# Optimization experiments

Hardware: AMD Instinct MI355X
Metric: run time of the kernel (lower is better)

The kernel has to match this reference:

```python
import jax, jax.numpy as jnp
import numpy as np
import math

L = 12      # n_layer (alternating adaptive True/False)
H = 8       # n_head
C = 256     # n_embd
DH = C // H # head dim = 32
BS = 828    # block_size
T = 827     # seq len after dropping last token
VOCAB = 16384
CAM = 30
IMG = 256


def get_sinusoid(n_position, d_hid):
    pos = np.arange(n_position)[:, None].astype(np.float64)
    hid = np.arange(d_hid)[None, :]
    angle = pos / np.power(10000.0, 2.0 * (hid // 2) / d_hid)
    table = np.zeros_like(angle)
    table[:, 0::2] = np.sin(angle[:, 0::2])
    table[:, 1::2] = np.cos(angle[:, 1::2])
    return jnp.asarray(table[None], jnp.float32)  # [1, n_position, d_hid]


def layer_norm(x, w, b):
    m = x.mean(-1, keepdims=True)
    v = ((x - m) ** 2).mean(-1, keepdims=True)
    return (x - m) * jax.lax.rsqrt(v + 1e-5) * w + b


def setup_inputs() -> dict:
    key = jax.random.key(0)
    ks = iter(jax.random.split(key, 64))
    nrm = lambda shape, s=1.0: jax.random.normal(next(ks), shape, jnp.float32) * s
    B = 4
    inp = {
        'dc_emb': nrm((B, 572, C)),
        'z_emb': nrm((B, 256, C)),
        'p1': nrm((B, CAM)),
        'p2': nrm((B, CAM)),
        'p3': nrm((B, CAM)),
        'frame_emb': nrm((1, 256, C), 0.02),
        'camera_emb': nrm((1, 30, C), 0.02),
        'time_emb': get_sinusoid(BS, C),
        'loc_W1': nrm((2 * CAM, CAM), 0.02), 'loc_b1': jnp.zeros((2 * CAM,)),
        'loc_W2': nrm((IMG * IMG, 2 * CAM), 0.02), 'loc_b2': jnp.zeros((IMG * IMG,)),
        'ln1_w': jnp.ones((L, C)), 'ln1_b': jnp.zeros((L, C)),
        'Wq': nrm((L, C, C), 0.02), 'bq': jnp.zeros((L, C)),
        'Wk': nrm((L, C, C), 0.02), 'bk': jnp.zeros((L, C)),
        'Wv': nrm((L, C, C), 0.02), 'bv': jnp.zeros((L, C)),
        'Wo': nrm((L, C, C), 0.02), 'bo': jnp.zeros((L, C)),
        'ln2_w': jnp.ones((L, C)), 'ln2_b': jnp.zeros((L, C)),
        'W1': nrm((L, 4 * C, C), 0.02), 'b1': jnp.zeros((L, 4 * C)),
        'W2': nrm((L, C, 4 * C), 0.02), 'b2': jnp.zeros((L, C)),
        'lnf_w': jnp.ones((C,)), 'lnf_b': jnp.zeros((C,)),
        'head_W': nrm((VOCAB, C), 0.02),
    }
    return inp


def _forward(dc_emb, z_emb, p1, p2, p3, frame_emb, camera_emb, time_emb,
             loc_W1, loc_b1, loc_W2, loc_b2,
             ln1_w, ln1_b, Wq, bq, Wk, bk, Wv, bv, Wo, bo,
             ln2_w, ln2_b, W1, b1, W2, b2, lnf_w, lnf_b, head_W):
    B = dc_emb.shape[0]
    scale = 1.0 / math.sqrt(DH)

    # AdaptiveAttention bias h: [B, 1, BS, BS] with three 256x256 learned blocks
    def locality(p):
        z = jax.nn.gelu(p @ loc_W1.T + loc_b1, approximate=False)
        z = z @ loc_W2.T + loc_b2
        return z.reshape(B, IMG, IMG)

    h = jnp.zeros((B, 1, BS, BS), dc_emb.dtype)
    h = h.at[:, 0, 285:541, 0:256].set(locality(p1))
    h = h.at[:, 0, 571:827, 0:256].set(locality(p2))
    h = h.at[:, 0, 571:827, 286:542].set(locality(p3))
    h = h[:, :, :T, :T]

    # token + role + time embeddings
    tok = jnp.concatenate([dc_emb, z_emb], axis=1)[:, :-1, :]  # [B, T, C]
    role = jnp.concatenate([frame_emb, camera_emb, frame_emb, camera_emb, frame_emb], axis=1)[:, :T, :]
    x = tok + role + time_emb[:, :T, :]

    causal = jnp.tril(jnp.ones((T, T), bool))  # [T, T]

    for i in range(L):
        adaptive = (i % 2 == 0)
        xn = layer_norm(x, ln1_w[i], ln1_b[i])
        q = (xn @ Wq[i].T + bq[i]).reshape(B, T, H, DH)
        k = (xn @ Wk[i].T + bk[i]).reshape(B, T, H, DH)
        v = (xn @ Wv[i].T + bv[i]).reshape(B, T, H, DH)
        att = jnp.einsum('bqhd,bkhd->bhqk', q, k) * scale
        if adaptive:
            att = att + h
        att = jnp.where(causal, att, -jnp.inf)
        att = jax.nn.softmax(att, axis=-1)
        y = jnp.einsum('bhqk,bkhd->bqhd', att, v).reshape(B, T, C)
        x = x + y @ Wo[i].T + bo[i]
        xn2 = layer_norm(x, ln2_w[i], ln2_b[i])
        x = x + jax.nn.gelu(xn2 @ W1[i].T + b1[i], approximate=False) @ W2[i].T + b2[i]

    x = layer_norm(x, lnf_w, lnf_b)
    logits = x @ head_W.T  # [B, T, VOCAB]
    return logits


def reference(dc_emb, z_emb, p1, p2, p3, frame_emb, camera_emb, time_emb,
              loc_W1, loc_b1, loc_W2, loc_b2,
              ln1_w, ln1_b, Wq, bq, Wk, bk, Wv, bv, Wo, bo,
              ln2_w, ln2_b, W1, b1, W2, b2, lnf_w, lnf_b, head_W):
    return _forward(dc_emb, z_emb, p1, p2, p3, frame_emb, camera_emb, time_emb,
                    loc_W1, loc_b1, loc_W2, loc_b2,
                    ln1_w, ln1_b, Wq, bq, Wk, bk, Wv, bv, Wo, bo,
                    ln2_w, ln2_b, W1, b1, W2, b2, lnf_w, lnf_b, head_W)
```

## Files before the change

### kernel.cpp

```cpp
#include <hip/hip_runtime.h>
#include <hip/hip_bf16.h>
#include <math.h>

#define T_LEN 827
#define M_ROWS 3308
#define NLAYER 12

typedef __attribute__((ext_vector_type(4))) float f32x4;
typedef __attribute__((ext_vector_type(8))) short bf16x8;

__device__ __forceinline__ float gelu_f(float x) {
    return 0.5f * x * (1.0f + erff(x * 0.70710678118654752440f));
}

__device__ __forceinline__ short f2bf_s(float x) {
    __hip_bfloat16 h = __float2bfloat16(x);
    return *reinterpret_cast<short*>(&h);
}

__global__ void cvt_kernel(const float* __restrict__ in, __hip_bfloat16* __restrict__ out, int n4) {
    int i = blockIdx.x * blockDim.x + threadIdx.x;
    if (i >= n4) return;
    float4 v = reinterpret_cast<const float4*>(in)[i];
    out[4*i+0] = __float2bfloat16(v.x);
    out[4*i+1] = __float2bfloat16(v.y);
    out[4*i+2] = __float2bfloat16(v.z);
    out[4*i+3] = __float2bfloat16(v.w);
}

__global__ void prep_wqkv_kernel(const float* __restrict__ Wq, const float* __restrict__ Wk,
                                 const float* __restrict__ Wv, __hip_bfloat16* __restrict__ out) {
    int i = blockIdx.x * 256 + threadIdx.x;
    if (i >= 12*768*64) return;
    int el = i * 4;
    int layer = el / (768*256);
    int rem = el % (768*256);
    int row = rem >> 8, col = rem & 255;
    const float* src;
    float sc = 1.f;
    if (row < 256)      { src = Wq + ((size_t)layer*256 + row)*256 + col; sc = 0.17677669529663687f; }
    else if (row < 512) { src = Wk + ((size_t)layer*256 + (row-256))*256 + col; }
    else                { src = Wv + ((size_t)layer*256 + (row-512))*256 + col; }
    float4 v = *reinterpret_cast<const float4*>(src);
    out[el+0] = __float2bfloat16(v.x * sc);
    out[el+1] = __float2bfloat16(v.y * sc);
    out[el+2] = __float2bfloat16(v.z * sc);
    out[el+3] = __float2bfloat16(v.w * sc);
}

__global__ void prep_bqkv_kernel(const float* __restrict__ bq, const float* __restrict__ bk,
                                 const float* __restrict__ bv, float* __restrict__ out) {
    int i = blockIdx.x * 256 + threadIdx.x;
    if (i >= 12*768) return;
    int layer = i / 768, row = i % 768;
    float v;
    if (row < 256)      v = bq[layer*256 + row] * 0.17677669529663687f;
    else if (row < 512) v = bk[layer*256 + (row-256)];
    else                v = bv[layer*256 + (row-512)];
    out[i] = v;
}

__global__ void zero_kernel(float* __restrict__ p, int n) {
    for (int i = blockIdx.x * blockDim.x + threadIdx.x; i < n; i += gridDim.x * blockDim.x)
        p[i] = 0.f;
}

__global__ void loc_z1_kernel(const float* __restrict__ p1, const float* __restrict__ p2,
                              const float* __restrict__ p3, const float* __restrict__ W1,
                              const float* __restrict__ b1, float* __restrict__ z1) {
    for (int i = threadIdx.x; i < 720; i += 256) {
        int pi = i / 240, rem = i % 240, b = rem / 60, j = rem % 60;
        const float* p = (pi == 0) ? p1 : ((pi == 1) ? p2 : p3);
        float acc = b1[j];
        #pragma unroll
        for (int c = 0; c < 30; ++c) acc += p[b*30 + c] * W1[j*30 + c];
        z1[i] = gelu_f(acc);
    }
}

__global__ void h_fill_kernel(const float* __restrict__ z1, const float* __restrict__ W2,
                              const float* __restrict__ b2, float* __restrict__ h) {
    __shared__ float z[720];
    int tid = threadIdx.x;
    for (int i = tid; i < 720; i += 256) z[i] = z1[i];
    __syncthreads();
    int j = blockIdx.x * 256 + tid;
    float w[60];
    #pragma unroll
    for (int c = 0; c < 60; ++c) w[c] = W2[(size_t)j*60 + c];
    float bj = b2[j];
    int r = j >> 8, cc = j & 255;
    const int br[3] = {285, 571, 571};
    const int bc[3] = {0, 0, 286};
    #pragma unroll
    for (int pi = 0; pi < 3; ++pi) {
        for (int b = 0; b < 4; ++b) {
            float acc = bj;
            #pragma unroll
            for (int c = 0; c < 60; ++c) acc += z[pi*240 + b*60 + c] * w[c];
            h[(size_t)b*T_LEN*T_LEN + (size_t)(br[pi] + r)*T_LEN + bc[pi] + cc] = acc;
        }
    }
}

__global__ void init_x_kernel(const float* __restrict__ dc, const float* __restrict__ z,
                              const float* __restrict__ frame, const float* __restrict__ cam,
                              const float* __restrict__ timeE, float* __restrict__ x) {
    int idx = blockIdx.x * 256 + threadIdx.x;
    int m = idx >> 8, c = idx & 255;
    int b = m / T_LEN, t = m % T_LEN;
    float tok = (t < 572) ? dc[((size_t)b*572 + t)*256 + c]
                          : z[((size_t)b*256 + (t - 572))*256 + c];
    float role;
    if      (t < 256) role = frame[t*256 + c];
    else if (t < 286) role = cam[(t-256)*256 + c];
    else if (t < 542) role = frame[(t-286)*256 + c];
    else if (t < 572) role = cam[(t-542)*256 + c];
    else              role = frame[(t-572)*256 + c];
    x[idx] = tok + role + timeE[t*256 + c];
}

template<bool LN, bool RESID, bool OUTBF16>
__global__ __launch_bounds__(256) void gemm_k256(
    const float* __restrict__ xsrc, const float* __restrict__ lnw, const float* __restrict__ lnb,
    const __hip_bfloat16* __restrict__ Abf,
    const __hip_bfloat16* __restrict__ W, const float* __restrict__ bias,
    const float* __restrict__ resid, void* __restrict__ out, int M, int N)
{
    __shared__ __hip_bfloat16 As[64][264];
    __shared__ __hip_bfloat16 Bs[64][264];
    __shared__ float redS[4][64], redQ[4][64];
    const int tid = threadIdx.x;
    const int m0 = blockIdx.x * 64, n0 = blockIdx.y * 64;
    const int r = tid >> 2, sg = tid & 3;

    {
        const __hip_bfloat16* bsrc = W + (size_t)(n0 + r) * 256 + sg * 8;
        #pragma unroll
        for (int j = 0; j < 8; ++j)
            *reinterpret_cast<uint4*>(&Bs[r][sg*8 + j*32]) =
                *reinterpret_cast<const uint4*>(bsrc + j*32);
    }
    int gr = m0 + r; if (gr > M-1) gr = M-1;
    if constexpr (LN) {
        const float* src = xsrc + (size_t)gr * 256;
        float s = 0.f, q = 0.f;
        #pragma unroll
        for (int j = 0; j < 8; ++j) {
            int k = sg*8 + j*32;
            float4 a = *reinterpret_cast<const float4*>(src + k);
            float4 c4 = *reinterpret_cast<const float4*>(src + k + 4);
            s += a.x + a.y + a.z + a.w + c4.x + c4.y + c4.z + c4.w;
            q += a.x*a.x + a.y*a.y + a.z*a.z + a.w*a.w
               + c4.x*c4.x + c4.y*c4.y + c4.z*c4.z + c4.w*c4.w;
        }
        redS[sg][r] = s; redQ[sg][r] = q;
        __syncthreads();
        float mean = (redS[0][r] + redS[1][r] + redS[2][r] + redS[3][r]) * (1.f/256.f);
        float msq  = (redQ[0][r] + redQ[1][r] + redQ[2][r] + redQ[3][r]) * (1.f/256.f);
        float rstd = rsqrtf(msq - mean*mean + 1e-5f);
        #pragma unroll
        for (int j = 0; j < 8; ++j) {
            int k = sg*8 + j*32;
            float4 a = *reinterpret_cast<const float4*>(src + k);
            float4 c4 = *reinterpret_cast<const float4*>(src + k + 4);
            float v[8] = {a.x, a.y, a.z, a.w, c4.x, c4.y, c4.z, c4.w};
            bf16x8 pk;
            #pragma unroll
            for (int e = 0; e < 8; ++e)
                pk[e] = f2bf_s((v[e] - mean) * rstd * lnw[k+e] + lnb[k+e]);
            *reinterpret_cast<bf16x8*>(&As[r][k]) = pk;
        }
    } else {
        const __hip_bfloat16* asrc = Abf + (size_t)gr * 256 + sg * 8;
        #pragma unroll
        for (int j = 0; j < 8; ++j)
            *reinterpret_cast<uint4*>(&As[r][sg*8 + j*32]) =
                *reinterpret_cast<const uint4*>(asrc + j*32);
    }
    __syncthreads();

    const int wid = tid >> 6, lane = tid & 63;
    const int wm = wid >> 1, wn = wid & 1, c = lane & 15, g = lane >> 4;
    f32x4 acc[2][2];
    #pragma unroll
    for (int mi = 0; mi < 2; ++mi)
        #pragma unroll
        for (int ni = 0; ni < 2; ++ni)
            acc[mi][ni] = (f32x4){0.f, 0.f, 0.f, 0.f};

    #pragma unroll
    for (int kj = 0; kj < 8; ++kj) {
        bf16x8 a0 = *reinterpret_cast<const bf16x8*>(&As[wm*32 + c][kj*32 + g*8]);
        bf16x8 a1 = *reinterpret_cast<const bf16x8*>(&As[wm*32 + 16 + c][kj*32 + g*8]);
        bf16x8 b0 = *reinterpret_cast<const bf16x8*>(&Bs[wn*32 + c][kj*32 + g*8]);
        bf16x8 b1v = *reinterpret_cast<const bf16x8*>(&Bs[wn*32 + 16 + c][kj*32 + g*8]);
        acc[0][0] = __builtin_amdgcn_mfma_f32_16x16x32_bf16(a0, b0, acc[0][0], 0, 0, 0);
        acc[0][1] = __builtin_amdgcn_mfma_f32_16x16x32_bf16(a0, b1v, acc[0][1], 0, 0, 0);
        acc[1][0] = __builtin_amdgcn_mfma_f32_16x16x32_bf16(a1, b0, acc[1][0], 0, 0, 0);
        acc[1][1] = __builtin_amdgcn_mfma_f32_16x16x32_bf16(a1, b1v, acc[1][1], 0, 0, 0);
    }

    #pragma unroll
    for (int mi = 0; mi < 2; ++mi) {
        #pragma unroll
        for (int ni = 0; ni < 2; ++ni) {
            int n = n0 + wn*32 + ni*16 + c;
            float bb = bias ? bias[n] : 0.f;
            #pragma unroll
            for (int rg = 0; rg < 4; ++rg) {
                int m = m0 + wm*32 + mi*16 + g*4 + rg;
                if (m >= M) continue;
                float v = acc[mi][ni][rg] + bb;
                if (RESID) v += resid[(size_t)m*N + n];
                if (OUTBF16) ((__hip_bfloat16*)out)[(size_t)m*N + n] = __float2bfloat16(v);
                else         ((float*)out)[(size_t)m*N + n] = v;
            }
        }
    }
}

template<bool FINAL>
__global__ __launch_bounds__(512) void mlp_fused(
    float* __restrict__ x,
    const float* __restrict__ ln2w, const float* __restrict__ ln2b,
    const __hip_bfloat16* __restrict__ W1, const float* __restrict__ b1,
    const __hip_bfloat16* __restrict__ W2, const float* __restrict__ b2,
    const float* __restrict__ lnfw, const float* __restrict__ lnfb,
    __hip_bfloat16* __restrict__ xn)
{
    __shared__ __hip_bfloat16 As[32][264];
    __shared__ __hip_bfloat16 Ms[32][1044];
    const int tid = threadIdx.x;
    const int m0 = blockIdx.x * 32;
    const int w = tid >> 6, lane = tid & 63, c = lane & 15, g = lane >> 4;

    {
        int r = tid >> 4, p = tid & 15;
        int gr = m0 + r; if (gr > M_ROWS-1) gr = M_ROWS-1;
        const float* src = x + (size_t)gr*256 + p*16;
        float4 f0 = *reinterpret_cast<const float4*>(src);
        float4 f1 = *reinterpret_cast<const float4*>(src + 4);
        float4 f2 = *reinterpret_cast<const float4*>(src + 8);
        float4 f3 = *reinterpret_cast<const float4*>(src + 12);
        float vv[16] = {f0.x,f0.y,f0.z,f0.w, f1.x,f1.y,f1.z,f1.w,
                        f2.x,f2.y,f2.z,f2.w, f3.x,f3.y,f3.z,f3.w};
        float s = 0.f, q = 0.f;
        #pragma unroll
        for (int e = 0; e < 16; ++e) { s += vv[e]; q += vv[e]*vv[e]; }
        #pragma unroll
        for (int msk = 1; msk <= 8; msk <<= 1) { s += __shfl_xor(s, msk); q += __shfl_xor(q, msk); }
        float mean = s * (1.f/256.f);
        float rstd = rsqrtf(q*(1.f/256.f) - mean*mean + 1e-5f);
        bf16x8 pk0, pk1;
        #pragma unroll
        for (int e = 0; e < 8; ++e) {
            pk0[e] = f2bf_s((vv[e]   - mean)*rstd*ln2w[p*16+e]   + ln2b[p*16+e]);
            pk1[e] = f2bf_s((vv[8+e] - mean)*rstd*ln2w[p*16+8+e] + ln2b[p*16+8+e]);
        }
        *reinterpret_cast<bf16x8*>(&As[r][p*16])     = pk0;
        *reinterpret_cast<bf16x8*>(&As[r][p*16 + 8]) = pk1;
    }
    __syncthreads();

    #pragma unroll 1
    for (int ns = 0; ns < 8; ++ns) {
        int nb = w*128 + ns*16;
        const __hip_bfloat16* wrow = W1 + (size_t)(nb + c)*256 + g*8;
        f32x4 a0 = (f32x4){0.f,0.f,0.f,0.f}, a1 = (f32x4){0.f,0.f,0.f,0.f};
        #pragma unroll
        for (int kj = 0; kj < 8; ++kj) {
            bf16x8 bfrag = *reinterpret_cast<const bf16x8*>(wrow + kj*32);
            bf16x8 af0 = *reinterpret_cast<const bf16x8*>(&As[c][kj*32 + g*8]);
            bf16x8 af1 = *reinterpret_cast<const bf16x8*>(&As[16 + c][kj*32 + g*8]);
            a0 = __builtin_amdgcn_mfma_f32_16x16x32_bf16(af0, bfrag, a0, 0, 0, 0);
            a1 = __builtin_amdgcn_mfma_f32_16x16x32_bf16(af1, bfrag, a1, 0, 0, 0);
        }
        float bb = b1[nb + c];
        #pragma unroll
        for (int rg = 0; rg < 4; ++rg) {
            Ms[g*4 + rg][nb + c]      = __float2bfloat16(gelu_f(a0[rg] + bb));
            Ms[16 + g*4 + rg][nb + c] = __float2bfloat16(gelu_f(a1[rg] + bb));
        }
    }
    __syncthreads();

    f32x4 o[2][2];
    #pragma unroll
    for (int i = 0; i < 2; ++i)
        #pragma unroll
        for (int j = 0; j < 2; ++j)
            o[i][j] = (f32x4){0.f,0.f,0.f,0.f};
    #pragma unroll
    for (int ns2 = 0; ns2 < 2; ++ns2) {
        int nb = w*32 + ns2*16;
        const __hip_bfloat16* wrow = W2 + (size_t)(nb + c)*1024 + g*8;
        #pragma unroll
        for (int kj = 0; kj < 32; ++kj) {
            bf16x8 bfrag = *reinterpret_cast<const bf16x8*>(wrow + kj*32);
            bf16x8 af0 = *reinterpret_cast<const bf16x8*>(&Ms[c][kj*32 + g*8]);
            bf16x8 af1 = *reinterpret_cast<const bf16x8*>(&Ms[16 + c][kj*32 + g*8]);
            o[ns2][0] = __builtin_amdgcn_mfma_f32_16x16x32_bf16(af0, bfrag, o[ns2][0], 0, 0, 0);
            o[ns2][1] = __builtin_amdgcn_mfma_f32_16x16x32_bf16(af1, bfrag, o[ns2][1], 0, 0, 0);
        }
    }
    __syncthreads();

    float* xf = reinterpret_cast<float*>(&Ms[0][0]);
    #pragma unroll
    for (int ns2 = 0; ns2 < 2; ++ns2) {
        int nb = w*32 + ns2*16;
        float bb = b2[nb + c];
        #pragma unroll
        for (int mi = 0; mi < 2; ++mi) {
            #pragma unroll
            for (int rg = 0; rg < 4; ++rg) {
                int row = mi*16 + g*4 + rg;
                int gm = m0 + row;
                if (gm < M_ROWS) {
                    float v = o[ns2][mi][rg] + bb + x[(size_t)gm*256 + nb + c];
                    x[(size_t)gm*256 + nb + c] = v;
                    if (FINAL) xf[row*256 + nb + c] = v;
                }
            }
        }
    }

    if constexpr (FINAL) {
        __syncthreads();
        int r = tid >> 4, p = tid & 15;
        int gm = m0 + r;
        const float* src = xf + r*256 + p*16;
        float4 f0 = *reinterpret_cast<const float4*>(src);
        float4 f1 = *reinterpret_cast<const float4*>(src + 4);
        float4 f2 = *reinterpret_cast<const float4*>(src + 8);
        float4 f3 = *reinterpret_cast<const float4*>(src + 12);
        float vv[16] = {f0.x,f0.y,f0.z,f0.w, f1.x,f1.y,f1.z,f1.w,
                        f2.x,f2.y,f2.z,f2.w, f3.x,f3.y,f3.z,f3.w};
        float s = 0.f, q = 0.f;
        #pragma unroll
        for (int e = 0; e < 16; ++e) { s += vv[e]; q += vv[e]*vv[e]; }
        #pragma unroll
        for (int msk = 1; msk <= 8; msk <<= 1) { s += __shfl_xor(s, msk); q += __shfl_xor(q, msk); }
        float mean = s * (1.f/256.f);
        float rstd = rsqrtf(q*(1.f/256.f) - mean*mean + 1e-5f);
        if (gm < M_ROWS) {
            bf16x8 pk0, pk1;
            #pragma unroll
            for (int e = 0; e < 8; ++e) {
                pk0[e] = f2bf_s((vv[e]   - mean)*rstd*lnfw[p*16+e]   + lnfb[p*16+e]);
                pk1[e] = f2bf_s((vv[8+e] - mean)*rstd*lnfw[p*16+8+e] + lnfb[p*16+8+e]);
            }
            *reinterpret_cast<bf16x8*>(&xn[(size_t)gm*256 + p*16])     = pk0;
            *reinterpret_cast<bf16x8*>(&xn[(size_t)gm*256 + p*16 + 8]) = pk1;
        }
    }
}

template<int ADAPT>
__global__ __launch_bounds__(256) void attn_mfma_kernel(const __hip_bfloat16* __restrict__ qkv,
                                                        const float* __restrict__ hbuf,
                                                        __hip_bfloat16* __restrict__ y) {
    const int qi = blockIdx.x, hh = blockIdx.y, b = blockIdx.z;
    const int tid = threadIdx.x;
    const int w = tid >> 6, lane = tid & 63;
    const int c = lane & 15, g = lane >> 4;
    const int q0 = qi * 64;
    const int qw0 = q0 + w * 16;

    __shared__ short Ks[2][64][40];
    __shared__ short Vt[2][32][68];
    __shared__ short Pw[4][16][72];

    int qrow = qw0 + c; if (qrow > T_LEN-1) qrow = T_LEN-1;
    bf16x8 aq = *reinterpret_cast<const bf16x8*>(qkv + ((size_t)b*T_LEN + qrow)*768 + hh*32 + g*8);

    float m_r[4] = {-INFINITY, -INFINITY, -INFINITY, -INFINITY};
    float l_r[4] = {0.f, 0.f, 0.f, 0.f};
    f32x4 acc[2];
    acc[0] = (f32x4){0.f,0.f,0.f,0.f};
    acc[1] = (f32x4){0.f,0.f,0.f,0.f};

    const int nk = min(q0 + 64, T_LEN);
    const int nit = (nk + 63) >> 6;
    const int srow = tid >> 2;
    const int scol8 = (tid & 3) * 8;

    bf16x8 kreg, vreg;
    {
        int krow = srow; if (krow > T_LEN-1) krow = T_LEN-1;
        const __hip_bfloat16* base = qkv + ((size_t)b*T_LEN + krow)*768 + hh*32 + scol8;
        kreg = *reinterpret_cast<const bf16x8*>(base + 256);
        vreg = *reinterpret_cast<const bf16x8*>(base + 512);
    }

    for (int it = 0; it < nit; ++it) {
        const int bsel = it & 1;
        const int kb = it * 64;
        *reinterpret_cast<bf16x8*>(&Ks[bsel][srow][scol8]) = kreg;
        #pragma unroll
        for (int jj = 0; jj < 8; ++jj) Vt[bsel][scol8 + jj][srow] = vreg[jj];
        __syncthreads();
        if (it + 1 < nit) {
            int krow = kb + 64 + srow; if (krow > T_LEN-1) krow = T_LEN-1;
            const __hip_bfloat16* base = qkv + ((size_t)b*T_LEN + krow)*768 + hh*32 + scol8;
            kreg = *reinterpret_cast<const bf16x8*>(base + 256);
            vreg = *reinterpret_cast<const bf16x8*>(base + 512);
        }

        f32x4 sc4[4];
        #pragma unroll
        for (int j = 0; j < 4; ++j) {
            bf16x8 bk = *reinterpret_cast<const bf16x8*>(&Ks[bsel][j*16 + c][g*8]);
            sc4[j] = __builtin_amdgcn_mfma_f32_16x16x32_bf16(aq, bk, (f32x4){0.f,0.f,0.f,0.f}, 0, 0, 0);
        }

        float sv[4][4];
        #pragma unroll
        for (int j = 0; j < 4; ++j) {
            int kk = kb + j*16 + c;
            #pragma unroll
            for (int rg = 0; rg < 4; ++rg) {
                int qq = qw0 + g*4 + rg;
                bool valid = (qq < T_LEN) && (kk <= qq);
                float s = sc4[j][rg];
                if (ADAPT) s += valid ? hbuf[((size_t)b*T_LEN + qq)*T_LEN + kk] : 0.f;
                sv[j][rg] = valid ? s : -INFINITY;
            }
        }

        float sf[4];
        #pragma unroll
        for (int rg = 0; rg < 4; ++rg) {
            float m = fmaxf(fmaxf(sv[0][rg], sv[1][rg]), fmaxf(sv[2][rg], sv[3][rg]));
            #pragma unroll
            for (int msk = 1; msk <= 8; msk <<= 1) m = fmaxf(m, __shfl_xor(m, msk));
            float mn = fmaxf(m_r[rg], m);
            sf[rg] = __expf(m_r[rg] - mn);
            m_r[rg] = mn;
        }
        float p[4][4];
        #pragma unroll
        for (int rg = 0; rg < 4; ++rg) {
            float su = 0.f;
            #pragma unroll
            for (int j = 0; j < 4; ++j) {
                float e = __expf(sv[j][rg] - m_r[rg]);
                p[j][rg] = e;
                su += e;
            }
            #pragma unroll
            for (int msk = 1; msk <= 8; msk <<= 1) su += __shfl_xor(su, msk);
            l_r[rg] = l_r[rg] * sf[rg] + su;
            acc[0][rg] *= sf[rg];
            acc[1][rg] *= sf[rg];
        }

        #pragma unroll
        for (int j = 0; j < 4; ++j)
            #pragma unroll
            for (int rg = 0; rg < 4; ++rg)
                Pw[w][g*4 + rg][j*16 + c] = f2bf_s(p[j][rg]);

        #pragma unroll
        for (int kc = 0; kc < 2; ++kc) {
            bf16x8 ap = *reinterpret_cast<const bf16x8*>(&Pw[w][c][kc*32 + g*8]);
            #pragma unroll
            for (int dt = 0; dt < 2; ++dt) {
                bf16x8 bv = *reinterpret_cast<const bf16x8*>(&Vt[bsel][dt*16 + c][kc*32 + g*8]);
                acc[dt] = __builtin_amdgcn_mfma_f32_16x16x32_bf16(ap, bv, acc[dt], 0, 0, 0);
            }
        }
    }

    #pragma unroll
    for (int rg = 0; rg < 4; ++rg) {
        int qq = qw0 + g*4 + rg;
        if (qq >= T_LEN) continue;
        float inv = 1.f / l_r[rg];
        #pragma unroll
        for (int dt = 0; dt < 2; ++dt)
            y[((size_t)b*T_LEN + qq)*256 + hh*32 + dt*16 + c] = __float2bfloat16(acc[dt][rg] * inv);
    }
}

extern "C" void kernel_launch(void* const* d_in, const int* in_sizes, int n_in,
                              void* d_out, int out_size, void* d_ws, size_t ws_size,
                              hipStream_t stream) {
    const float* dc    = (const float*)d_in[0];
    const float* zemb  = (const float*)d_in[1];
    const float* p1    = (const float*)d_in[2];
    const float* p2    = (const float*)d_in[3];
    const float* p3    = (const float*)d_in[4];
    const float* frame = (const float*)d_in[5];
    const float* cam   = (const float*)d_in[6];
    const float* timeE = (const float*)d_in[7];
    const float* locW1 = (const float*)d_in[8];
    const float* locb1 = (const float*)d_in[9];
    const float* locW2 = (const float*)d_in[10];
    const float* locb2 = (const float*)d_in[11];
    const float* ln1w  = (const float*)d_in[12];
    const float* ln1b  = (const float*)d_in[13];
    const float* Wq    = (const float*)d_in[14];
    const float* bq    = (const float*)d_in[15];
    const float* Wk    = (const float*)d_in[16];
    const float* bk    = (const float*)d_in[17];
    const float* Wv    = (const float*)d_in[18];
    const float* bv    = (const float*)d_in[19];
    const float* Wo    = (const float*)d_in[20];
    const float* bo    = (const float*)d_in[21];
    const float* ln2w  = (const float*)d_in[22];
    const float* ln2b  = (const float*)d_in[23];
    const float* W1p   = (const float*)d_in[24];
    const float* b1p   = (const float*)d_in[25];
    const float* W2p   = (const float*)d_in[26];
    const float* b2p   = (const float*)d_in[27];
    const float* lnfw  = (const float*)d_in[28];
    const float* lnfb  = (const float*)d_in[29];
    const float* headW = (const float*)d_in[30];

    char* wsb = (char*)d_ws;
    size_t off = 0;
    auto alloc = [&](size_t bytes) -> char* {
        char* p = wsb + off;
        off += (bytes + 255) & ~(size_t)255;
        return p;
    };
    __hip_bfloat16* wqkv_bf = (__hip_bfloat16*)alloc(12ull*768*256*2);
    float*          bqkv    = (float*)alloc(12ull*768*4);
    __hip_bfloat16* wo_bf = (__hip_bfloat16*)alloc(12ull*65536*2);
    __hip_bfloat16* w1_bf = (__hip_bfloat16*)alloc(12ull*262144*2);
    __hip_bfloat16* w2_bf = (__hip_bfloat16*)alloc(12ull*262144*2);
    __hip_bfloat16* wh_bf = (__hip_bfloat16*)alloc(16384ull*256*2);
    float* hbuf = (float*)alloc(4ull*T_LEN*T_LEN*4);
    float* x    = (float*)alloc((size_t)M_ROWS*256*4);
    __hip_bfloat16* xn   = (__hip_bfloat16*)alloc((size_t)M_ROWS*256*2);
    __hip_bfloat16* qkvb = (__hip_bfloat16*)alloc((size_t)M_ROWS*768*2);
    __hip_bfloat16* yb   = (__hip_bfloat16*)alloc((size_t)M_ROWS*256*2);
    float* z1   = (float*)alloc(720*4);

    prep_wqkv_kernel<<<(12*768*64 + 255)/256, 256, 0, stream>>>(Wq, Wk, Wv, wqkv_bf);
    prep_bqkv_kernel<<<36, 256, 0, stream>>>(bq, bk, bv, bqkv);
    cvt_kernel<<<768, 256, 0, stream>>>(Wo, wo_bf, 196608);
    cvt_kernel<<<3072, 256, 0, stream>>>(W1p, w1_bf, 786432);
    cvt_kernel<<<3072, 256, 0, stream>>>(W2p, w2_bf, 786432);
    cvt_kernel<<<4096, 256, 0, stream>>>(headW, wh_bf, 1048576);

    loc_z1_kernel<<<1, 256, 0, stream>>>(p1, p2, p3, locW1, locb1, z1);
    zero_kernel<<<2048, 256, 0, stream>>>(hbuf, 4*T_LEN*T_LEN);
    h_fill_kernel<<<256, 256, 0, stream>>>(z1, locW2, locb2, hbuf);

    init_x_kernel<<<M_ROWS, 256, 0, stream>>>(dc, zemb, frame, cam, timeE, x);

    dim3 gqkv(52, 12);
    dim3 goproj(52, 4);
    dim3 gattn(13, 8, 4);

    for (int i = 0; i < NLAYER; ++i) {
        gemm_k256<true,false,true><<<gqkv, 256, 0, stream>>>(
            x, ln1w + i*256, ln1b + i*256, nullptr,
            wqkv_bf + (size_t)i*196608, bqkv + i*768, nullptr, qkvb, M_ROWS, 768);
        if (i % 2 == 0) attn_mfma_kernel<1><<<gattn, 256, 0, stream>>>(qkvb, hbuf, yb);
        else            attn_mfma_kernel<0><<<gattn, 256, 0, stream>>>(qkvb, hbuf, yb);
        gemm_k256<false,true,false><<<goproj, 256, 0, stream>>>(
            nullptr, nullptr, nullptr, yb,
            wo_bf + (size_t)i*65536, bo + i*256, x, x, M_ROWS, 256);
        if (i == NLAYER-1)
            mlp_fused<true><<<104, 512, 0, stream>>>(
                x, ln2w + i*256, ln2b + i*256,
                w1_bf + (size_t)i*262144, b1p + i*1024,
                w2_bf + (size_t)i*262144, b2p + i*256, lnfw, lnfb, xn);
        else
            mlp_fused<false><<<104, 512, 0, stream>>>(
                x, ln2w + i*256, ln2b + i*256,
                w1_bf + (size_t)i*262144, b1p + i*1024,
                w2_bf + (size_t)i*262144, b2p + i*256, nullptr, nullptr, nullptr);
    }

    gemm_k256<false,false,false><<<dim3(52, 256), 256, 0, stream>>>(
        nullptr, nullptr, nullptr, xn, wh_bf, nullptr, nullptr, (float*)d_out, M_ROWS, 16384);
}
```

Measured before the change: 1.183 ms.

## Split attention along keys with merge pass, store bias in bf16, fuse next-layer LN

Attention is split into key chunks of up to 256 keys (28 work items per batch-head instead of 13 query blocks). Each chunk writes partial outputs and running max/sum, and a separate merge kernel combines them, which is meant to balance causal work and raise occupancy. The adaptive bias buffer is stored in bf16 to halve its memory traffic. The MLP kernel now always emits the next layer's LN1-normalised bf16 activations, so the QKV GEMM no longer recomputes layernorm. The cost is an extra launch per layer, fp32 partial round-trips through memory, and bf16 rounding of the bias.

```diff
diff --git a/kernel.cpp b/kernel.cpp
--- a/kernel.cpp
+++ b/kernel.cpp
@@ -79,7 +79,7 @@
 }
 
 __global__ void h_fill_kernel(const float* __restrict__ z1, const float* __restrict__ W2,
-                              const float* __restrict__ b2, float* __restrict__ h) {
+                              const float* __restrict__ b2, __hip_bfloat16* __restrict__ h) {
     __shared__ float z[720];
     int tid = threadIdx.x;
     for (int i = tid; i < 720; i += 256) z[i] = z1[i];
@@ -98,7 +98,7 @@
             float acc = bj;
             #pragma unroll
             for (int c = 0; c < 60; ++c) acc += z[pi*240 + b*60 + c] * w[c];
-            h[(size_t)b*T_LEN*T_LEN + (size_t)(br[pi] + r)*T_LEN + bc[pi] + cc] = acc;
+            h[(size_t)b*T_LEN*T_LEN + (size_t)(br[pi] + r)*T_LEN + bc[pi] + cc] = __float2bfloat16(acc);
         }
     }
 }
@@ -120,6 +120,31 @@
     x[idx] = tok + role + timeE[t*256 + c];
 }
 
+__global__ __launch_bounds__(256) void ln_kernel(const float* __restrict__ x,
+                                                 const float* __restrict__ w,
+                                                 const float* __restrict__ b,
+                                                 __hip_bfloat16* __restrict__ out) {
+    int row = blockIdx.x, tid = threadIdx.x;
+    float v = x[(size_t)row*256 + tid];
+    float s = v;
+    #pragma unroll
+    for (int off = 32; off; off >>= 1) s += __shfl_down(s, off);
+    __shared__ float red[4];
+    if ((tid & 63) == 0) red[tid >> 6] = s;
+    __syncthreads();
+    float mean = (red[0] + red[1] + red[2] + red[3]) * (1.f/256.f);
+    float d = v - mean;
+    float s2 = d * d;
+    #pragma unroll
+    for (int off = 32; off; off >>= 1) s2 += __shfl_down(s2, off);
+    __shared__ float red2[4];
+    if ((tid & 63) == 0) red2[tid >> 6] = s2;
+    __syncthreads();
+    float var = (red2[0] + red2[1] + red2[2] + red2[3]) * (1.f/256.f);
+    float rs = rsqrtf(var + 1e-5f);
+    out[(size_t)row*256 + tid] = __float2bfloat16(d * rs * w[tid] + b[tid]);
+}
+
 template<bool LN, bool RESID, bool OUTBF16>
 __global__ __launch_bounds__(256) void gemm_k256(
     const float* __restrict__ xsrc, const float* __restrict__ lnw, const float* __restrict__ lnb,
@@ -220,13 +245,12 @@
     }
 }
 
-template<bool FINAL>
 __global__ __launch_bounds__(512) void mlp_fused(
     float* __restrict__ x,
     const float* __restrict__ ln2w, const float* __restrict__ ln2b,
     const __hip_bfloat16* __restrict__ W1, const float* __restrict__ b1,
     const __hip_bfloat16* __restrict__ W2, const float* __restrict__ b2,
-    const float* __restrict__ lnfw, const float* __restrict__ lnfb,
+    const float* __restrict__ lnow, const float* __restrict__ lnob,
     __hip_bfloat16* __restrict__ xn)
 {
     __shared__ __hip_bfloat16 As[32][264];
@@ -320,14 +344,14 @@
                 if (gm < M_ROWS) {
                     float v = o[ns2][mi][rg] + bb + x[(size_t)gm*256 + nb + c];
                     x[(size_t)gm*256 + nb + c] = v;
-                    if (FINAL) xf[row*256 + nb + c] = v;
+                    xf[row*256 + nb + c] = v;
                 }
             }
         }
     }
-
-    if constexpr (FINAL) {
-        __syncthreads();
+    __syncthreads();
+
+    {
         int r = tid >> 4, p = tid & 15;
         int gm = m0 + r;
         const float* src = xf + r*256 + p*16;
@@ -348,8 +372,8 @@
             bf16x8 pk0, pk1;
             #pragma unroll
             for (int e = 0; e < 8; ++e) {
-                pk0[e] = f2bf_s((vv[e]   - mean)*rstd*lnfw[p*16+e]   + lnfb[p*16+e]);
-                pk1[e] = f2bf_s((vv[8+e] - mean)*rstd*lnfw[p*16+8+e] + lnfb[p*16+8+e]);
+                pk0[e] = f2bf_s((vv[e]   - mean)*rstd*lnow[p*16+e]   + lnob[p*16+e]);
+                pk1[e] = f2bf_s((vv[8+e] - mean)*rstd*lnow[p*16+8+e] + lnob[p*16+8+e]);
             }
             *reinterpret_cast<bf16x8*>(&xn[(size_t)gm*256 + p*16])     = pk0;
             *reinterpret_cast<bf16x8*>(&xn[(size_t)gm*256 + p*16 + 8]) = pk1;
@@ -358,14 +382,28 @@
 }
 
 template<int ADAPT>
-__global__ __launch_bounds__(256) void attn_mfma_kernel(const __hip_bfloat16* __restrict__ qkv,
-                                                        const float* __restrict__ hbuf,
-                                                        __hip_bfloat16* __restrict__ y) {
-    const int qi = blockIdx.x, hh = blockIdx.y, b = blockIdx.z;
+__global__ __launch_bounds__(256) void attn_split_kernel(const __hip_bfloat16* __restrict__ qkv,
+                                                         const __hip_bfloat16* __restrict__ hbuf,
+                                                         float* __restrict__ pacc,
+                                                         float* __restrict__ pml) {
+    const int fi = blockIdx.x, hh = blockIdx.y, b = blockIdx.z;
+    int qi = 0;
+    while (qi < 12) {
+        int n1 = qi + 1;
+        int bn = n1 + (n1 > 4 ? n1 - 4 : 0) + (n1 > 8 ? n1 - 8 : 0);
+        if (fi < bn) break;
+        ++qi;
+    }
+    const int base = qi + (qi > 4 ? qi - 4 : 0) + (qi > 8 ? qi - 8 : 0);
+    const int ck = fi - base;
+    const int q0 = qi * 64;
+    const int kstart = ck * 256;
+    const int kend = min(q0 + 64, T_LEN);
+    const int nit = min(4, (kend - kstart + 63) >> 6);
+
     const int tid = threadIdx.x;
     const int w = tid >> 6, lane = tid & 63;
     const int c = lane & 15, g = lane >> 4;
-    const int q0 = qi * 64;
     const int qw0 = q0 + w * 16;
 
     __shared__ short Ks[2][64][40];
@@ -381,31 +419,29 @@
     acc[0] = (f32x4){0.f,0.f,0.f,0.f};
     acc[1] = (f32x4){0.f,0.f,0.f,0.f};
 
-    const int nk = min(q0 + 64, T_LEN);
-    const int nit = (nk + 63) >> 6;
     const int srow = tid >> 2;
     const int scol8 = (tid & 3) * 8;
 
     bf16x8 kreg, vreg;
     {
-        int krow = srow; if (krow > T_LEN-1) krow = T_LEN-1;
-        const __hip_bfloat16* base = qkv + ((size_t)b*T_LEN + krow)*768 + hh*32 + scol8;
-        kreg = *reinterpret_cast<const bf16x8*>(base + 256);
-        vreg = *reinterpret_cast<const bf16x8*>(base + 512);
+        int krow = kstart + srow; if (krow > T_LEN-1) krow = T_LEN-1;
+        const __hip_bfloat16* gbase = qkv + ((size_t)b*T_LEN + krow)*768 + hh*32 + scol8;
+        kreg = *reinterpret_cast<const bf16x8*>(gbase + 256);
+        vreg = *reinterpret_cast<const bf16x8*>(gbase + 512);
     }
 
     for (int it = 0; it < nit; ++it) {
         const int bsel = it & 1;
-        const int kb = it * 64;
+        const int kb = kstart + it * 64;
         *reinterpret_cast<bf16x8*>(&Ks[bsel][srow][scol8]) = kreg;
         #pragma unroll
         for (int jj = 0; jj < 8; ++jj) Vt[bsel][scol8 + jj][srow] = vreg[jj];
         __syncthreads();
         if (it + 1 < nit) {
             int krow = kb + 64 + srow; if (krow > T_LEN-1) krow = T_LEN-1;
-            const __hip_bfloat16* base = qkv + ((size_t)b*T_LEN + krow)*768 + hh*32 + scol8;
-            kreg = *reinterpret_cast<const bf16x8*>(base + 256);
-            vreg = *reinterpret_cast<const bf16x8*>(base + 512);
+            const __hip_bfloat16* gbase = qkv + ((size_t)b*T_LEN + krow)*768 + hh*32 + scol8;
+            kreg = *reinterpret_cast<const bf16x8*>(gbase + 256);
+            vreg = *reinterpret_cast<const bf16x8*>(gbase + 512);
         }
 
         f32x4 sc4[4];
@@ -424,7 +460,7 @@
                 int qq = qw0 + g*4 + rg;
                 bool valid = (qq < T_LEN) && (kk <= qq);
                 float s = sc4[j][rg];
-                if (ADAPT) s += valid ? hbuf[((size_t)b*T_LEN + qq)*T_LEN + kk] : 0.f;
+                if (ADAPT) s += valid ? __bfloat162float(hbuf[((size_t)b*T_LEN + qq)*T_LEN + kk]) : 0.f;
                 sv[j][rg] = valid ? s : -INFINITY;
             }
         }
@@ -473,14 +509,43 @@
         }
     }
 
+    const int slot = (b*8 + hh)*28 + fi;
+    float* paccs = pacc + (size_t)slot * 2048;
     #pragma unroll
     for (int rg = 0; rg < 4; ++rg) {
-        int qq = qw0 + g*4 + rg;
+        int row = w*16 + g*4 + rg;
+        paccs[row*32 + c]      = acc[0][rg];
+        paccs[row*32 + 16 + c] = acc[1][rg];
+        if (c == 0) {
+            pml[(size_t)slot*128 + row*2]     = m_r[rg];
+            pml[(size_t)slot*128 + row*2 + 1] = l_r[rg];
+        }
+    }
+}
+
+__global__ __launch_bounds__(256) void attn_merge_kernel(const float* __restrict__ pacc,
+                                                         const float* __restrict__ pml,
+                                                         __hip_bfloat16* __restrict__ y) {
+    const int qi = blockIdx.x, hh = blockIdx.y, b = blockIdx.z;
+    const int nc = qi/4 + 1;
+    const int base = qi + (qi > 4 ? qi - 4 : 0) + (qi > 8 ? qi - 8 : 0);
+    const int slot0 = (b*8 + hh)*28 + base;
+    const int t = threadIdx.x, d = t & 31, r8 = t >> 5;
+    for (int rr = r8; rr < 64; rr += 8) {
+        int qq = qi*64 + rr;
         if (qq >= T_LEN) continue;
-        float inv = 1.f / l_r[rg];
-        #pragma unroll
-        for (int dt = 0; dt < 2; ++dt)
-            y[((size_t)b*T_LEN + qq)*256 + hh*32 + dt*16 + c] = __float2bfloat16(acc[dt][rg] * inv);
+        float M = -INFINITY;
+        for (int cc2 = 0; cc2 < nc; ++cc2)
+            M = fmaxf(M, pml[(size_t)(slot0+cc2)*128 + rr*2]);
+        float L = 0.f, o = 0.f;
+        for (int cc2 = 0; cc2 < nc; ++cc2) {
+            float mm = pml[(size_t)(slot0+cc2)*128 + rr*2];
+            float ll = pml[(size_t)(slot0+cc2)*128 + rr*2 + 1];
+            float sc = __expf(mm - M);
+            L += sc * ll;
+            o += sc * pacc[(size_t)(slot0+cc2)*2048 + rr*32 + d];
+        }
+        y[((size_t)b*T_LEN + qq)*256 + hh*32 + d] = __float2bfloat16(o / L);
     }
 }
 
@@ -532,11 +597,13 @@
     __hip_bfloat16* w1_bf = (__hip_bfloat16*)alloc(12ull*262144*2);
     __hip_bfloat16* w2_bf = (__hip_bfloat16*)alloc(12ull*262144*2);
     __hip_bfloat16* wh_bf = (__hip_bfloat16*)alloc(16384ull*256*2);
-    float* hbuf = (float*)alloc(4ull*T_LEN*T_LEN*4);
+    __hip_bfloat16* hbuf = (__hip_bfloat16*)alloc(4ull*T_LEN*T_LEN*2);
     float* x    = (float*)alloc((size_t)M_ROWS*256*4);
     __hip_bfloat16* xn   = (__hip_bfloat16*)alloc((size_t)M_ROWS*256*2);
     __hip_bfloat16* qkvb = (__hip_bfloat16*)alloc((size_t)M_ROWS*768*2);
     __hip_bfloat16* yb   = (__hip_bfloat16*)alloc((size_t)M_ROWS*256*2);
+    float* pacc = (float*)alloc(32ull*28*2048*4);
+    float* pml  = (float*)alloc(32ull*28*128*4);
     float* z1   = (float*)alloc(720*4);
 
     prep_wqkv_kernel<<<(12*768*64 + 255)/256, 256, 0, stream>>>(Wq, Wk, Wv, wqkv_bf);
@@ -547,34 +614,33 @@
     cvt_kernel<<<4096, 256, 0, stream>>>(headW, wh_bf, 1048576);
 
     loc_z1_kernel<<<1, 256, 0, stream>>>(p1, p2, p3, locW1, locb1, z1);
-    zero_kernel<<<2048, 256, 0, stream>>>(hbuf, 4*T_LEN*T_LEN);
+    zero_kernel<<<2048, 256, 0, stream>>>((float*)hbuf, (4*T_LEN*T_LEN)/2);
     h_fill_kernel<<<256, 256, 0, stream>>>(z1, locW2, locb2, hbuf);
 
     init_x_kernel<<<M_ROWS, 256, 0, stream>>>(dc, zemb, frame, cam, timeE, x);
+    ln_kernel<<<M_ROWS, 256, 0, stream>>>(x, ln1w, ln1b, xn);
 
     dim3 gqkv(52, 12);
     dim3 goproj(52, 4);
-    dim3 gattn(13, 8, 4);
+    dim3 gsplit(28, 8, 4);
+    dim3 gmerge(13, 8, 4);
 
     for (int i = 0; i < NLAYER; ++i) {
-        gemm_k256<true,false,true><<<gqkv, 256, 0, stream>>>(
-            x, ln1w + i*256, ln1b + i*256, nullptr,
+        gemm_k256<false,false,true><<<gqkv, 256, 0, stream>>>(
+            nullptr, nullptr, nullptr, xn,
             wqkv_bf + (size_t)i*196608, bqkv + i*768, nullptr, qkvb, M_ROWS, 768);
-        if (i % 2 == 0) attn_mfma_kernel<1><<<gattn, 256, 0, stream>>>(qkvb, hbuf, yb);
-        else            attn_mfma_kernel<0><<<gattn, 256, 0, stream>>>(qkvb, hbuf, yb);
+        if (i % 2 == 0) attn_split_kernel<1><<<gsplit, 256, 0, stream>>>(qkvb, hbuf, pacc, pml);
+        else            attn_split_kernel<0><<<gsplit, 256, 0, stream>>>(qkvb, hbuf, pacc, pml);
+        attn_merge_kernel<<<gmerge, 256, 0, stream>>>(pacc, pml, yb);
         gemm_k256<false,true,false><<<goproj, 256, 0, stream>>>(
             nullptr, nullptr, nullptr, yb,
             wo_bf + (size_t)i*65536, bo + i*256, x, x, M_ROWS, 256);
-        if (i == NLAYER-1)
-            mlp_fused<true><<<104, 512, 0, stream>>>(
-                x, ln2w + i*256, ln2b + i*256,
-                w1_bf + (size_t)i*262144, b1p + i*1024,
-                w2_bf + (size_t)i*262144, b2p + i*256, lnfw, lnfb, xn);
-        else
-            mlp_fused<false><<<104, 512, 0, stream>>>(
-                x, ln2w + i*256, ln2b + i*256,
-                w1_bf + (size_t)i*262144, b1p + i*1024,
-                w2_bf + (size_t)i*262144, b2p + i*256, nullptr, nullptr, nullptr);
+        const float* lnow = (i == NLAYER-1) ? lnfw : (ln1w + (i+1)*256);
+        const float* lnob = (i == NLAYER-1) ? lnfb : (ln1b + (i+1)*256);
+        mlp_fused<<<104, 512, 0, stream>>>(
+            x, ln2w + i*256, ln2b + i*256,
+            w1_bf + (size_t)i*262144, b1p + i*1024,
+            w2_bf + (size_t)i*262144, b2p + i*256, lnow, lnob, xn);
     }
 
     gemm_k256<false,false,false><<<dim3(52, 256), 256, 0, stream>>>(
```

Result: slower. 1.354 ms (+14.5%).
